# Optimization experiments

Measured on AMD Instinct MI355X. Metric: run time of the kernel, lower is better.

The kernel has to match this reference:

```python
import jax, jax.numpy as jnp
import numpy as np

NT = 16          # nt_states
TS = 48          # t_states
T = NT + TS      # total states
B, N = 4, 24     # batch, sentence length
HUGE = 1.0e9


def setup_inputs():
    key = jax.random.key(0)
    k1, k2, k3 = jax.random.split(key, 3)
    unary_scores = jax.nn.log_softmax(jax.random.normal(k1, (B, N, T), jnp.float32), axis=-1)
    rule = jax.random.normal(k2, (B, NT, N, T, T, 2), jnp.float32)
    rule_scores = jax.nn.log_softmax(rule.reshape(B, NT, N, -1), axis=-1).reshape(B, NT, N, T, T, 2)
    root_scores = jax.nn.log_softmax(jax.random.normal(k3, (B, NT), jnp.float32), axis=-1)
    return {"unary_scores": unary_scores, "rule_scores": rule_scores, "root_scores": root_scores}


def _lse(x, axes):
    return jax.nn.logsumexp(x, axis=axes)


def _inside(unary_scores, rule_scores, root_scores):
    Bv, Nv, Tt = unary_scores.shape
    nt = rule_scores.shape[1]
    dt = unary_scores.dtype
    R = jnp.moveaxis(rule_scores, 5, 0)            # (D, B, Tparent, H, TL, TR)

    # beta[b,l,r,t,h]: headed inside chart; betau[b,l,r,t]: head-summed chart
    beta = jnp.full((Bv, Nv + 1, Nv + 1, Tt, Nv), -HUGE, dt)
    betau = jnp.full((Bv, Nv + 1, Nv + 1, Tt), -HUGE, dt)

    # width-1 spans: only terminal states (word_span_slice = nt:T, nt_emission=False)
    ks = np.arange(Nv)
    st = np.arange(nt, Tt)
    beta = beta.at[:, ks[:, None], ks[:, None] + 1, st[None, :], ks[:, None]].set(0.0)
    betau = betau.at[:, ks[:, None], ks[:, None] + 1, st[None, :]].set(
        unary_scores[:, ks[:, None], st[None, :]])

    nts = np.arange(nt)
    for W in range(2, Nv + 1):
        L = Nv - W + 1
        ls = np.arange(L)
        rs = ls + W
        hidx = ls[:, None] + np.arange(W)          # (L, W) absolute head positions

        def width_body(beta, betau, R, unary_scores, W=W, ls=ls, rs=rs, hidx=hidx):
            def chartH(la, ra, s0, s1):            # (B, L, S, W)
                x = beta[:, la, ra, s0:s1, :]
                return jnp.take_along_axis(x, hidx[None, :, None, :], axis=3)

            def chartU(la, ra, s0, s1):            # (B, L, S)
                return betau[:, la, ra, s0:s1]

            def rwin(d, a0, a1, c0, c1):           # (B, L, nt, W, A, C)
                r = R[d][:, :, hidx, a0:a1, c0:c1]
                return jnp.transpose(r, (0, 2, 1, 3, 4, 5))

            def comb(xH, yU, xU, yH, z0, z1):
                # D=0: head from left child; D=1: head from right child.
                # logsumexp over TL, TR and both directions -> (B, L, nt, W)
                left = (jnp.transpose(xH, (0, 1, 3, 2))[:, :, None, :, :, None]
                        + yU[:, :, None, None, None, :] + z0)
                right = (xU[:, :, None, None, :, None]
                         + jnp.transpose(yH, (0, 1, 3, 2))[:, :, None, :, None, :] + z1)
                return jnp.logaddexp(_lse(left, (-2, -1)), _lse(right, (-2, -1)))

            c0, c1 = (nt, Tt) if W == 2 else (0, nt)
            # split at l+1: left child is a single terminal
            tmp = comb(chartH(ls, ls + 1, nt, Tt), chartU(ls + 1, rs, c0, c1),
                       chartU(ls, ls + 1, nt, Tt), chartH(ls + 1, rs, c0, c1),
                       rwin(0, nt, Tt, c0, c1), rwin(1, nt, Tt, c0, c1))
            if W >= 3:
                # split at r-1: right child is a single terminal
                tmp = jnp.logaddexp(tmp, comb(
                    chartH(ls, rs - 1, 0, nt), chartU(rs - 1, rs, nt, Tt),
                    chartU(ls, rs - 1, 0, nt), chartH(rs - 1, rs, nt, Tt),
                    rwin(0, 0, nt, nt, Tt), rwin(1, 0, nt, nt, Tt)))
            if W >= 4:
                # interior splits: both children are nonterminal spans
                z0 = rwin(0, 0, nt, 0, nt)
                z1 = rwin(1, 0, nt, 0, nt)
                for wl in range(2, W - 1):
                    s = ls + wl
                    tmp = jnp.logaddexp(tmp, comb(
                        chartH(ls, s, 0, nt), chartU(s, rs, 0, nt),
                        chartU(ls, s, 0, nt), chartH(s, rs, 0, nt), z0, z1))
            # add head-word emission under the parent NT; sum heads for betau
            uw = jnp.transpose(unary_scores[:, hidx, :nt], (0, 1, 3, 2))  # (B,L,nt,W)
            return tmp, _lse(tmp + uw, -1)

        tmp, tmpu = jax.checkpoint(width_body)(beta, betau, R, unary_scores)
        beta = beta.at[:, ls[:, None, None], rs[:, None, None],
                       nts[None, :, None], hidx[:, None, :]].set(tmp)
        betau = betau.at[:, ls[:, None], rs[:, None], nts[None, :]].set(tmpu)

    return jax.nn.logsumexp(betau[:, 0, Nv, :nt] + root_scores, axis=-1)  # log Z, (B,)


_inside_jit = jax.jit(_inside)


def reference(unary_scores, rule_scores, root_scores):
    return _inside_jit(unary_scores, rule_scores, root_scores)
```

## Files before the change

kernel.cpp:

```cpp
#include <hip/hip_runtime.h>
#include <cstddef>

#define Bv 4
#define Nv 24
#define NTv 16
#define Tv 64
#define NP 25
#define NEGF (-1e30f)

typedef __attribute__((ext_vector_type(8))) short short8v;
typedef __attribute__((ext_vector_type(4))) float f32x4;
union FragU { unsigned u[4]; short8v s; };

#define BETAA_OFF 0
#define BETAU_OFF 960000
#define RNT_OFF   1120000
#define T0_OFF    1906432
#define T1_OFF    2496256
#define T0L_OFF   3086080
#define T1R_OFF   3110656
#define D0_OFF    3135232
#define D1_OFF    3136768
#define EU_OFF    3138304
#define CELLF_OFF 3142912
#define WS_NEED   3145412

__device__ __forceinline__ void publish(float* p, float v) {
  __hip_atomic_store(p, v, __ATOMIC_RELAXED, __HIP_MEMORY_SCOPE_AGENT);
}

__device__ __forceinline__ unsigned packbf2(float lo, float hi) {
  unsigned bl = __float_as_uint(lo), bh = __float_as_uint(hi);
  bl = (bl + 0x7FFFu + ((bl >> 16) & 1u)) >> 16;
  bh = (bh + 0x7FFFu + ((bh >> 16) & 1u)) >> 16;
  return (bh << 16) | bl;
}

__global__ void init_kernel(const float* __restrict__ unary, float* __restrict__ betau,
                            float* __restrict__ Eu, int* __restrict__ cellF) {
  int t = blockIdx.x * blockDim.x + threadIdx.x;
  if (t < Bv * NP * NP) cellF[t] = 0;
  if (t >= Bv * Nv * 48) return;
  int i = t % 48, kk = (t / 48) % Nv, b = t / (48 * Nv);
  float u = unary[(size_t)(b * Nv + kk) * Tv + 16 + i];
  betau[((size_t)(b * NP + kk) * NP + (kk + 1)) * Tv + 16 + i] = u;
  Eu[(size_t)(b * Nv + kk) * 48 + i] = __expf(u);
}

__global__ __launch_bounds__(256) void prep_kernel(
    const float* __restrict__ rule, const float* __restrict__ Eu,
    unsigned* __restrict__ RNTh, float* __restrict__ T0, float* __restrict__ T1,
    float* __restrict__ T0L, float* __restrict__ T1R,
    float* __restrict__ D0, float* __restrict__ D1) {
  const int h = blockIdx.x, A = blockIdx.y, b = blockIdx.z;
  const int t = threadIdx.x;
  __shared__ float er0[64 * 65];
  __shared__ float er1[64 * 65];
  __shared__ float E[24 * 48];
  __shared__ float red[256];

  for (int i = t; i < 24 * 48; i += 256) E[i] = Eu[(size_t)b * (24 * 48) + i];
  const float* rb = rule + (size_t)((b * NTv + A) * Nv + h) * 8192;
#pragma unroll
  for (int i = 0; i < 8; ++i) {
    int lin = i * 1024 + t * 4;
    float4 v = *(const float4*)(rb + lin);
    int sL = lin >> 7, rem = (lin & 127) >> 1;
    er0[sL * 65 + rem] = __expf(v.x);
    er1[sL * 65 + rem] = __expf(v.y);
    er0[sL * 65 + rem + 1] = __expf(v.z);
    er1[sL * 65 + rem + 1] = __expf(v.w);
  }
  __syncthreads();
  {
    unsigned* dst0 = RNTh + (((size_t)(b * 2 + 0) * Nv + h) * NTv + A) * 128;
    unsigned* dst1 = RNTh + (((size_t)(b * 2 + 1) * Nv + h) * NTv + A) * 128;
    if (t < 128) {
      int sL = t >> 3, sRp = t & 7;
      dst0[t] = packbf2(er0[sL * 65 + 2 * sRp], er0[sL * 65 + 2 * sRp + 1]);
    } else {
      int t2 = t - 128;
      int sL = t2 >> 3, sRp = t2 & 7;
      dst1[t2] = packbf2(er1[sL * 65 + 2 * sRp], er1[sL * 65 + 2 * sRp + 1]);
    }
  }
  for (int o = t; o < 384; o += 256) {
    int p = o >> 4, sL = o & 15;
    const float* Ep = E + p * 48;
    const float* r0 = er0 + sL * 65 + 16;
    float acc = 0.f;
#pragma unroll 8
    for (int j = 0; j < 48; ++j) acc += Ep[j] * r0[j];
    T0[(((size_t)(b * Nv + h) * Nv + p) * NTv + sL) * NTv + A] = acc;
  }
  for (int o = t; o < 384; o += 256) {
    int p = o >> 4, sR = o & 15;
    const float* Ep = E + p * 48;
    float acc = 0.f;
#pragma unroll 8
    for (int i = 0; i < 48; ++i) acc += Ep[i] * er1[(16 + i) * 65 + sR];
    T1[(((size_t)(b * Nv + h) * Nv + p) * NTv + sR) * NTv + A] = acc;
  }
  if (t < 16) {
    float acc = 0.f;
    for (int i = 0; i < 48; ++i) acc += er0[(16 + i) * 65 + t];
    T0L[((size_t)(b * Nv + h) * NTv + t) * NTv + A] = acc;
  } else if (t < 32) {
    int sL = t - 16;
    float acc = 0.f;
    for (int j = 0; j < 48; ++j) acc += er1[sL * 65 + 16 + j];
    T1R[((size_t)(b * Nv + h) * NTv + sL) * NTv + A] = acc;
  }
  float acc0 = 0.f, acc1 = 0.f;
  const int hp = (h + 1 < 24) ? h + 1 : 0, hm = (h >= 1) ? h - 1 : 0;
  for (int e = t; e < 2304; e += 256) {
    int i = e / 48, j = e % 48;
    float r0 = er0[(16 + i) * 65 + 16 + j];
    float r1 = er1[(16 + i) * 65 + 16 + j];
    acc0 += E[hp * 48 + j] * r0;
    acc1 += E[hm * 48 + i] * r1;
  }
  red[t] = acc0;
  __syncthreads();
  if (t < 64) {
    float s = red[t] + red[t + 64] + red[t + 128] + red[t + 192];
#pragma unroll
    for (int off = 32; off; off >>= 1) s += __shfl_xor(s, off, 64);
    if (t == 0 && h <= 22) D0[((size_t)b * Nv + h) * NTv + A] = s;
  }
  __syncthreads();
  red[t] = acc1;
  __syncthreads();
  if (t < 64) {
    float s = red[t] + red[t + 64] + red[t + 128] + red[t + 192];
#pragma unroll
    for (int off = 32; off; off >>= 1) s += __shfl_xor(s, off, 64);
    if (t == 0 && h >= 1) D1[((size_t)b * Nv + (h - 1)) * NTv + A] = s;
  }
}

__device__ __forceinline__ void edge_dot(float v0, float v1, float v2, float v3,
                                         const float* Tb, float& sh, float& S) {
  float mx = fmaxf(fmaxf(v0, v1), fmaxf(v2, v3));
  mx = fmaxf(mx, __shfl_xor(mx, 1, 64));
  mx = fmaxf(mx, __shfl_xor(mx, 2, 64));
  float dot = __expf(v0 - mx) * Tb[0] + __expf(v1 - mx) * Tb[16] +
              __expf(v2 - mx) * Tb[32] + __expf(v3 - mx) * Tb[48];
  dot += __shfl_xor(dot, 1, 64);
  dot += __shfl_xor(dot, 2, 64);
  sh = mx;
  S = dot;
}

__global__ __launch_bounds__(768) void width_all_kernel(
    const float* __restrict__ unary, float* __restrict__ betaA, float* __restrict__ betau,
    const unsigned* __restrict__ RNTh, const float* __restrict__ T0, const float* __restrict__ T1,
    const float* __restrict__ T0L, const float* __restrict__ T1R,
    const float* __restrict__ D0, const float* __restrict__ D1,
    const float* __restrict__ root, float* __restrict__ out, int* __restrict__ cellF) {
  const int rr = blockIdx.x, b = blockIdx.y;
  const int r = rr + 2;
  const int tid = threadIdx.x;
  int* flagb = cellF + b * (NP * NP);

  __shared__ float chartC[23][384];
  __shared__ float buC[23][16];
  __shared__ float U0[24 * 256], U1[24 * 256];
  __shared__ float pM[2 * 24 * 16], pS[2 * 24 * 16];
  __shared__ float sTmp[16 * 24];

  const int wv = tid >> 6, lane = tid & 63;
  const int sym = lane & 15;
  const int mBlk = (lane >> 4) * 8;

  for (int i = 0; i <= r - 2; ++i) {
    const int l = r - 2 - i;
    const int W = r - l;

    if (W >= 3) {
      if (tid < W - 3) {
        const int m = l + 2 + tid;
        while (__hip_atomic_load(&flagb[l * NP + m], __ATOMIC_RELAXED,
                                 __HIP_MEMORY_SCOPE_AGENT) == 0)
          __builtin_amdgcn_s_sleep(1);
      }
      __syncthreads();
    }

    float Gp[4];
#pragma unroll
    for (int pi = 0; pi < 4; ++pi) {
      const int p = wv + 12 * pi;
      if (p < 2 * W) {
        const int hh = p >> 1, d = p & 1, hcol = l + hh;
        int mst, cnt;
        if (d) { mst = l + 2; cnt = min(l + hh, r - 2) - mst + 1; }
        else   { mst = max(l + hh + 1, l + 2); cnt = (r - 2) - mst + 1; }
        if (cnt < 0) cnt = 0;
        float* Ua = (d ? U1 : U0) + hh * 256;
        if (cnt == 0) {
#pragma unroll
          for (int reg = 0; reg < 4; ++reg)
            Ua[((lane >> 4) * 4 + reg) * 16 + sym] = 0.f;
          Gp[pi] = -2e30f;
        } else {
          float Lv[8], Rv[8];
          if (d) {
            const size_t lb = ((size_t)(b * NP + l) * NP + mst) * Tv + sym;
#pragma unroll
            for (int j = 0; j < 8; ++j) {
              int mi = mBlk + j;
              Lv[j] = (mi < cnt) ? betau[lb + (size_t)mi * Tv] : NEGF;
              Rv[j] = (mi < cnt) ? chartC[mst + mi][hcol * 16 + sym] : NEGF;
            }
          } else {
            const size_t lb = ((size_t)(b * NP + l) * NP + mst) * 384 + hcol * 16 + sym;
#pragma unroll
            for (int j = 0; j < 8; ++j) {
              int mi = mBlk + j;
              Lv[j] = (mi < cnt) ? betaA[lb + (size_t)mi * 384] : NEGF;
              Rv[j] = (mi < cnt) ? buC[mst + mi][sym] : NEGF;
            }
          }
          float mxL = NEGF, mxR = NEGF;
#pragma unroll
          for (int j = 0; j < 8; ++j) { mxL = fmaxf(mxL, Lv[j]); mxR = fmaxf(mxR, Rv[j]); }
#pragma unroll
          for (int off = 1; off < 64; off <<= 1) {
            mxL = fmaxf(mxL, __shfl_xor(mxL, off, 64));
            mxR = fmaxf(mxR, __shfl_xor(mxR, off, 64));
          }
          FragU fa, fb;
#pragma unroll
          for (int jj = 0; jj < 4; ++jj) {
            int m0i = mBlk + 2 * jj, m1i = m0i + 1;
            float e0 = (m0i < cnt) ? __expf(Lv[2 * jj] - mxL) : 0.f;
            float e1 = (m1i < cnt) ? __expf(Lv[2 * jj + 1] - mxL) : 0.f;
            fa.u[jj] = packbf2(e0, e1);
            float f0 = (m0i < cnt) ? __expf(Rv[2 * jj] - mxR) : 0.f;
            float f1 = (m1i < cnt) ? __expf(Rv[2 * jj + 1] - mxR) : 0.f;
            fb.u[jj] = packbf2(f0, f1);
          }
          f32x4 z = {0.f, 0.f, 0.f, 0.f};
          f32x4 dU = __builtin_amdgcn_mfma_f32_16x16x32_bf16(fa.s, fb.s, z, 0, 0, 0);
#pragma unroll
          for (int reg = 0; reg < 4; ++reg)
            Ua[((lane >> 4) * 4 + reg) * 16 + sym] = dU[reg];
          Gp[pi] = mxL + mxR;
        }
      }
    }

    if (W >= 3) {
      while (__hip_atomic_load(&flagb[l * NP + (r - 1)], __ATOMIC_RELAXED,
                               __HIP_MEMORY_SCOPE_AGENT) == 0)
        __builtin_amdgcn_s_sleep(1);
    }

#pragma unroll
    for (int pi = 0; pi < 4; ++pi) {
      const int p = wv + 12 * pi;
      if (p < 2 * W) {
        const int hh = p >> 1, d = p & 1, h = l + hh;
        const float* Ua = (d ? U1 : U0) + hh * 256;
        const unsigned* Rb = RNTh + (((size_t)(b * 2 + d) * Nv + h) * NTv + sym) * 128;
        f32x4 acc4 = {0.f, 0.f, 0.f, 0.f};
#pragma unroll
        for (int kk = 0; kk < 8; ++kk) {
          uint4 ar = *(const uint4*)(Rb + kk * 16 + (lane >> 4) * 4);
          FragU fa, fb;
          fa.u[0] = ar.x; fa.u[1] = ar.y; fa.u[2] = ar.z; fa.u[3] = ar.w;
          if (sym == 0) {
            const float* up = Ua + kk * 32 + mBlk;
#pragma unroll
            for (int jj = 0; jj < 4; ++jj) fb.u[jj] = packbf2(up[2 * jj], up[2 * jj + 1]);
          } else {
            fb.u[0] = 0; fb.u[1] = 0; fb.u[2] = 0; fb.u[3] = 0;
          }
          acc4 = __builtin_amdgcn_mfma_f32_16x16x32_bf16(fa.s, fb.s, acc4, 0, 0, 0);
        }
        const int A = lane >> 2, q = lane & 3;
        const int src = (A >> 2) << 4;
        float c0 = __shfl(acc4[0], src, 64);
        float c1 = __shfl(acc4[1], src, 64);
        float c2 = __shfl(acc4[2], src, 64);
        float c3 = __shfl(acc4[3], src, 64);
        const int sel = A & 3;
        float acc = (sel == 0) ? c0 : (sel == 1) ? c1 : (sel == 2) ? c2 : c3;
        float Mi = Gp[pi];
        float sh2 = NEGF, S2 = 0.f, sh3 = NEGF, S3 = 0.f;
        if (W >= 3) {
          if (d == 0) {
            if (hh < W - 1) {
              const float* Tb = T0 + (((size_t)(b * Nv + h) * Nv + (r - 1)) * NTv + 4 * q) * NTv + A;
              float4 e4 = *(const float4*)(betaA +
                  ((size_t)(b * NP + l) * NP + (r - 1)) * 384 + (size_t)h * 16 + 4 * q);
              edge_dot(e4.x, e4.y, e4.z, e4.w, Tb, sh2, S2);
            }
            if (hh == 0) {
              const float* Tb = T0L + ((size_t)(b * Nv + l) * NTv + 4 * q) * NTv + A;
              const float* u4 = &buC[l + 1][4 * q];
              edge_dot(u4[0], u4[1], u4[2], u4[3], Tb, sh3, S3);
            }
          } else {
            if (hh >= 1) {
              const float* Tb = T1 + (((size_t)(b * Nv + h) * Nv + l) * NTv + 4 * q) * NTv + A;
              const float* e4 = &chartC[l + 1][h * 16 + 4 * q];
              edge_dot(e4[0], e4[1], e4[2], e4[3], Tb, sh2, S2);
            }
            if (hh == W - 1) {
              const float* Tb = T1R + ((size_t)(b * Nv + (r - 1)) * NTv + 4 * q) * NTv + A;
              float4 u4 = *(const float4*)(betau +
                  ((size_t)(b * NP + l) * NP + (r - 1)) * Tv + 4 * q);
              edge_dot(u4.x, u4.y, u4.z, u4.w, Tb, sh3, S3);
            }
          }
        } else {
          if (d == 0 && hh == 0) { sh2 = 0.f; S2 = D0[((size_t)b * Nv + l) * NTv + A]; }
          if (d == 1 && hh == 1) { sh2 = 0.f; S2 = D1[((size_t)b * Nv + l) * NTv + A]; }
        }
        float Mf = fmaxf(Mi, fmaxf(sh2, sh3));
        float Sf = acc * __expf(Mi - Mf) + S2 * __expf(sh2 - Mf) + S3 * __expf(sh3 - Mf);
        if (q == 0) {
          pM[(d * 24 + hh) * 16 + A] = Mf;
          pS[(d * 24 + hh) * 16 + A] = Sf;
        }
      }
    }
    __syncthreads();

    if (tid < 384) {
      int A2 = tid & 15, hh = tid >> 4;
      if (hh < W) {
        float M0 = pM[(0 * 24 + hh) * 16 + A2], S0 = pS[(0 * 24 + hh) * 16 + A2];
        float M1 = pM[(1 * 24 + hh) * 16 + A2], S1 = pS[(1 * 24 + hh) * 16 + A2];
        float nm = fmaxf(M0, M1);
        float s = S0 * __expf(M0 - nm) + S1 * __expf(M1 - nm);
        float val = nm + __logf(s);
        publish(&betaA[((size_t)(b * NP + l) * NP + r) * 384 + (l + hh) * 16 + A2], val);
        chartC[l][(l + hh) * 16 + A2] = val;
        sTmp[A2 * 24 + hh] = val + unary[(size_t)(b * Nv + (l + hh)) * Tv + A2];
      }
    }
    __syncthreads();
    if (tid < 16) {
      float mx = NEGF;
      for (int x = 0; x < W; ++x) mx = fmaxf(mx, sTmp[tid * 24 + x]);
      float s = 0.f;
      for (int x = 0; x < W; ++x) s += __expf(sTmp[tid * 24 + x] - mx);
      float val = mx + __logf(s);
      publish(&betau[((size_t)(b * NP + l) * NP + r) * Tv + tid], val);
      buC[l][tid] = val;
    }
    if (tid == 0) {
      asm volatile("s_waitcnt vmcnt(0)" ::: "memory");
      __hip_atomic_store(&flagb[l * NP + r], 1, __ATOMIC_RELAXED,
                         __HIP_MEMORY_SCOPE_AGENT);
    }
  }

  if (rr == 22) {
    __syncthreads();
    if (tid == 0) {
      float vals[NTv];
      float mx = NEGF;
#pragma unroll
      for (int A = 0; A < NTv; ++A) {
        float v = buC[0][A] + root[b * NTv + A];
        vals[A] = v;
        mx = fmaxf(mx, v);
      }
      float s = 0.f;
#pragma unroll
      for (int A = 0; A < NTv; ++A) s += __expf(vals[A] - mx);
      out[b] = mx + __logf(s);
    }
  }
}

__global__ __launch_bounds__(768) void width_kernel_fb(
    const float* __restrict__ unary, const float* __restrict__ rule,
    float* __restrict__ betaA, float* __restrict__ betau, int W) {
  const int l = blockIdx.x, b = blockIdx.y;
  const int r = l + W;
  const int tid = threadIdx.x;
  const int sub = tid & 1;
  const int pid = tid >> 1;
  const int A = pid & 15;
  const int hh = pid >> 4;
  const int h = l + hh;
  const bool act = (hh < W);
  const int sA = tid & 15, sH = tid >> 4;

  __shared__ float sER0[48], sEL1[48];
  __shared__ float sCL0[16 * 24], sCR1[16 * 24];
  __shared__ float sMaxL0[24], sMaxR1[24];
  __shared__ float sShR0, sShL1;
  __shared__ float sTmp[16 * 24];

  float runM = NEGF, runS = 0.f;
  for (int m = l + 1; m < r; ++m) {
    const int wl = m - l, wr = r - m;
    if (tid < 64) {
      const int n = (wr == 1) ? 48 : 16, s0 = (wr == 1) ? 16 : 0;
      float v = (tid < n) ? betau[(size_t)((b * NP + m) * NP + r) * Tv + s0 + tid] : NEGF;
      float mx = v;
#pragma unroll
      for (int off = 32; off; off >>= 1) mx = fmaxf(mx, __shfl_xor(mx, off, 64));
      if (tid == 0) sShR0 = mx;
      if (tid < n) sER0[tid] = v - mx;
    } else if (tid < 128) {
      const int j = tid - 64;
      const int n = (wl == 1) ? 48 : 16, s0 = (wl == 1) ? 16 : 0;
      float v = (j < n) ? betau[(size_t)((b * NP + l) * NP + m) * Tv + s0 + j] : NEGF;
      float mx = v;
#pragma unroll
      for (int off = 32; off; off >>= 1) mx = fmaxf(mx, __shfl_xor(mx, off, 64));
      if (j == 0) sShL1 = mx;
      if (j < n) sEL1[j] = v - mx;
    }
    if (tid < 384) {
      if (wl > 1 && sH < wl) {
        float v = betaA[(size_t)((b * NP + l) * NP + m) * 384 + sA * Nv + (l + sH)];
        float mx = v;
#pragma unroll
        for (int off = 8; off; off >>= 1) mx = fmaxf(mx, __shfl_xor(mx, off, 16));
        if (sA == 0) sMaxL0[sH] = mx;
        sCL0[sA * Nv + sH] = v - mx;
      }
      if (wr > 1 && sH >= wl && sH < W) {
        float v = betaA[(size_t)((b * NP + m) * NP + r) * 384 + sA * Nv + (l + sH)];
        float mx = v;
#pragma unroll
        for (int off = 8; off; off >>= 1) mx = fmaxf(mx, __shfl_xor(mx, off, 16));
        if (sA == 0) sMaxR1[sH] = mx;
        sCR1[sA * Nv + sH] = v - mx;
      }
    }
    __syncthreads();
    if (act) {
      if (hh < wl && (wl > 1 || hh == 0)) {
        const int nL = (wl == 1) ? 48 : 16, sL0 = (wl == 1) ? 16 : 0;
        const int nR = (wr == 1) ? 48 : 16, sR0 = (wr == 1) ? 16 : 0;
        const float shift = ((wl == 1) ? 0.f : sMaxL0[hh]) + sShR0;
        float part = 0.f;
        const float* rb = rule + (size_t)(((b * NTv + A) * Nv + h) * Tv) * Tv * 2;
        for (int i = sub; i < nL; i += 2) {
          const float cl = (wl == 1) ? 0.f : sCL0[i * Nv + hh];
          const float* rp = rb + (size_t)(sL0 + i) * Tv * 2 + sR0 * 2;
#pragma unroll 8
          for (int j = 0; j < nR; ++j) part += __expf(cl + sER0[j] + rp[j * 2]);
        }
        float nm = fmaxf(runM, shift);
        runS = runS * __expf(runM - nm) + part * __expf(shift - nm);
        runM = nm;
      }
      if (hh >= wl && (wr > 1 || hh == W - 1)) {
        const int nL = (wl == 1) ? 48 : 16, sL0 = (wl == 1) ? 16 : 0;
        const int nR = (wr == 1) ? 48 : 16, sR0 = (wr == 1) ? 16 : 0;
        const float shift = sShL1 + ((wr == 1) ? 0.f : sMaxR1[hh]);
        float part = 0.f;
        const float* rb = rule + (size_t)(((b * NTv + A) * Nv + h) * Tv) * Tv * 2 + 1;
        for (int i = sub; i < nL; i += 2) {
          const float el = sEL1[i];
          const float* rp = rb + (size_t)(sL0 + i) * Tv * 2 + sR0 * 2;
#pragma unroll 8
          for (int j = 0; j < nR; ++j) {
            const float cr = (wr == 1) ? 0.f : sCR1[j * Nv + hh];
            part += __expf(el + cr + rp[j * 2]);
          }
        }
        float nm = fmaxf(runM, shift);
        runS = runS * __expf(runM - nm) + part * __expf(shift - nm);
        runM = nm;
      }
    }
    __syncthreads();
  }
  if (act) {
    float om = __shfl_xor(runM, 1, 64);
    float os = __shfl_xor(runS, 1, 64);
    float nm = fmaxf(runM, om);
    float s = runS * __expf(runM - nm) + os * __expf(om - nm);
    if (sub == 0) {
      float val = nm + __logf(s);
      betaA[(size_t)((b * NP + l) * NP + r) * 384 + A * Nv + h] = val;
      sTmp[A * Nv + hh] = val + unary[(b * Nv + h) * Tv + A];
    }
  }
  __syncthreads();
  if (tid < 16) {
    float mx = NEGF;
    for (int x = 0; x < W; ++x) mx = fmaxf(mx, sTmp[tid * Nv + x]);
    float s = 0.f;
    for (int x = 0; x < W; ++x) s += __expf(sTmp[tid * Nv + x] - mx);
    betau[(size_t)((b * NP + l) * NP + r) * Tv + tid] = mx + __logf(s);
  }
}

__global__ void final_kernel(const float* __restrict__ betau, const float* __restrict__ root,
                             float* __restrict__ out) {
  int b = threadIdx.x;
  if (b < Bv) {
    float vals[NTv];
    float mx = NEGF;
#pragma unroll
    for (int A = 0; A < NTv; ++A) {
      float v = betau[(size_t)((b * NP + 0) * NP + Nv) * Tv + A] + root[b * NTv + A];
      vals[A] = v;
      mx = fmaxf(mx, v);
    }
    float s = 0.f;
#pragma unroll
    for (int A = 0; A < NTv; ++A) s += __expf(vals[A] - mx);
    out[b] = mx + __logf(s);
  }
}

extern "C" void kernel_launch(void* const* d_in, const int* in_sizes, int n_in,
                              void* d_out, int out_size, void* d_ws, size_t ws_size,
                              hipStream_t stream) {
  (void)in_sizes; (void)n_in; (void)out_size;
  const float* unary = (const float*)d_in[0];
  const float* rule  = (const float*)d_in[1];
  const float* root  = (const float*)d_in[2];
  float* out = (float*)d_out;
  float* ws = (float*)d_ws;
  float* betaA = ws + BETAA_OFF;
  float* betau = ws + BETAU_OFF;
  const bool fast = ws_size >= (size_t)WS_NEED * sizeof(float);

  if (fast) {
    unsigned* RNTh = (unsigned*)(ws + RNT_OFF);
    float* T0  = ws + T0_OFF;
    float* T1  = ws + T1_OFF;
    float* T0L = ws + T0L_OFF;
    float* T1R = ws + T1R_OFF;
    float* D0  = ws + D0_OFF;
    float* D1  = ws + D1_OFF;
    float* Eu  = ws + EU_OFF;
    int* cellF = (int*)(ws + CELLF_OFF);
    init_kernel<<<(Bv * Nv * 48 + 255) / 256, 256, 0, stream>>>(unary, betau, Eu, cellF);
    prep_kernel<<<dim3(24, 16, 4), 256, 0, stream>>>(rule, Eu, RNTh, T0, T1, T0L, T1R, D0, D1);
    void* args[] = {(void*)&unary, (void*)&betaA, (void*)&betau, (void*)&RNTh,
                    (void*)&T0, (void*)&T1, (void*)&T0L, (void*)&T1R,
                    (void*)&D0, (void*)&D1, (void*)&root, (void*)&out, (void*)&cellF};
    hipLaunchCooperativeKernel((const void*)width_all_kernel, dim3(Nv - 1, Bv), dim3(768),
                               args, 0, stream);
  } else {
    float* Eu = ws + BETAU_OFF + 160000;
    int* prog = (int*)(ws + BETAU_OFF + 160000 + 4608);
    init_kernel<<<(Bv * Nv * 48 + 255) / 256, 256, 0, stream>>>(unary, betau, Eu, prog);
    for (int W = 2; W <= Nv; ++W) {
      dim3 grid(Nv - W + 1, Bv);
      width_kernel_fb<<<grid, 768, 0, stream>>>(unary, rule, betaA, betau, W);
    }
    final_kernel<<<1, 64, 0, stream>>>(betau, root, out);
  }
}
```

Before: 406.7 us.

## Pair adjacent right-endpoint columns per block to share edge cells via LDS

Each block now processes two adjacent right-endpoint columns (r=2g+1 and r=2g+2) in an interleaved order instead of one column per block, cutting the grid from 23 to 12 blocks per batch. Column rB reads its edge cell (l, rB-1) directly from column rA's shared-memory chart, removing one cross-block flag poll and global reads on the dependency chain. The cost is half as many concurrent blocks and serialisation of the two columns' work inside one block, plus a larger shared-memory footprint.

```diff
diff --git a/kernel.cpp b/kernel.cpp
--- a/kernel.cpp
+++ b/kernel.cpp
@@ -152,221 +152,253 @@
   S = dot;
 }
 
+__device__ __forceinline__ void cell_body(
+    int b, int r, int l, int tid,
+    float (*chartOwn)[384], float (*buOwn)[16],
+    const float* eChart, const float* eBu, int edgePollIdx, int* flagb,
+    float* U0, float* U1, float* pM, float* pS, float* sTmp,
+    const float* __restrict__ unary, float* __restrict__ betaA, float* __restrict__ betau,
+    const unsigned* __restrict__ RNTh, const float* __restrict__ T0,
+    const float* __restrict__ T1, const float* __restrict__ T0L,
+    const float* __restrict__ T1R, const float* __restrict__ D0,
+    const float* __restrict__ D1) {
+  const int W = r - l;
+  const int wv = tid >> 6, lane = tid & 63;
+  const int sym = lane & 15;
+  const int mBlk = (lane >> 4) * 8;
+
+  if (W >= 3) {
+    if (tid < W - 3) {
+      const int m = l + 2 + tid;
+      while (__hip_atomic_load(&flagb[l * NP + m], __ATOMIC_RELAXED,
+                               __HIP_MEMORY_SCOPE_AGENT) == 0)
+        __builtin_amdgcn_s_sleep(1);
+    }
+    __syncthreads();
+  }
+
+  float Gp[4];
+#pragma unroll
+  for (int pi = 0; pi < 4; ++pi) {
+    const int p = wv + 12 * pi;
+    if (p < 2 * W) {
+      const int hh = p >> 1, d = p & 1, hcol = l + hh;
+      int mst, cnt;
+      if (d) { mst = l + 2; cnt = min(l + hh, r - 2) - mst + 1; }
+      else   { mst = max(l + hh + 1, l + 2); cnt = (r - 2) - mst + 1; }
+      if (cnt < 0) cnt = 0;
+      float* Ua = (d ? U1 : U0) + hh * 256;
+      if (cnt == 0) {
+#pragma unroll
+        for (int reg = 0; reg < 4; ++reg)
+          Ua[((lane >> 4) * 4 + reg) * 16 + sym] = 0.f;
+        Gp[pi] = -2e30f;
+      } else {
+        float Lv[8], Rv[8];
+        if (d) {
+          const size_t lb = ((size_t)(b * NP + l) * NP + mst) * Tv + sym;
+#pragma unroll
+          for (int j = 0; j < 8; ++j) {
+            int mi = mBlk + j;
+            Lv[j] = (mi < cnt) ? betau[lb + (size_t)mi * Tv] : NEGF;
+            Rv[j] = (mi < cnt) ? chartOwn[mst + mi][hcol * 16 + sym] : NEGF;
+          }
+        } else {
+          const size_t lb = ((size_t)(b * NP + l) * NP + mst) * 384 + hcol * 16 + sym;
+#pragma unroll
+          for (int j = 0; j < 8; ++j) {
+            int mi = mBlk + j;
+            Lv[j] = (mi < cnt) ? betaA[lb + (size_t)mi * 384] : NEGF;
+            Rv[j] = (mi < cnt) ? buOwn[mst + mi][sym] : NEGF;
+          }
+        }
+        float mxL = NEGF, mxR = NEGF;
+#pragma unroll
+        for (int j = 0; j < 8; ++j) { mxL = fmaxf(mxL, Lv[j]); mxR = fmaxf(mxR, Rv[j]); }
+#pragma unroll
+        for (int off = 1; off < 64; off <<= 1) {
+          mxL = fmaxf(mxL, __shfl_xor(mxL, off, 64));
+          mxR = fmaxf(mxR, __shfl_xor(mxR, off, 64));
+        }
+        FragU fa, fb;
+#pragma unroll
+        for (int jj = 0; jj < 4; ++jj) {
+          int m0i = mBlk + 2 * jj, m1i = m0i + 1;
+          float e0 = (m0i < cnt) ? __expf(Lv[2 * jj] - mxL) : 0.f;
+          float e1 = (m1i < cnt) ? __expf(Lv[2 * jj + 1] - mxL) : 0.f;
+          fa.u[jj] = packbf2(e0, e1);
+          float f0 = (m0i < cnt) ? __expf(Rv[2 * jj] - mxR) : 0.f;
+          float f1 = (m1i < cnt) ? __expf(Rv[2 * jj + 1] - mxR) : 0.f;
+          fb.u[jj] = packbf2(f0, f1);
+        }
+        f32x4 z = {0.f, 0.f, 0.f, 0.f};
+        f32x4 dU = __builtin_amdgcn_mfma_f32_16x16x32_bf16(fa.s, fb.s, z, 0, 0, 0);
+#pragma unroll
+        for (int reg = 0; reg < 4; ++reg)
+          Ua[((lane >> 4) * 4 + reg) * 16 + sym] = dU[reg];
+        Gp[pi] = mxL + mxR;
+      }
+    }
+  }
+
+  if (W >= 3 && edgePollIdx >= 0) {
+    while (__hip_atomic_load(&flagb[edgePollIdx], __ATOMIC_RELAXED,
+                             __HIP_MEMORY_SCOPE_AGENT) == 0)
+      __builtin_amdgcn_s_sleep(1);
+  }
+
+#pragma unroll
+  for (int pi = 0; pi < 4; ++pi) {
+    const int p = wv + 12 * pi;
+    if (p < 2 * W) {
+      const int hh = p >> 1, d = p & 1, h = l + hh;
+      const float* Ua = (d ? U1 : U0) + hh * 256;
+      const unsigned* Rb = RNTh + (((size_t)(b * 2 + d) * Nv + h) * NTv + sym) * 128;
+      f32x4 acc4 = {0.f, 0.f, 0.f, 0.f};
+#pragma unroll
+      for (int kk = 0; kk < 8; ++kk) {
+        uint4 ar = *(const uint4*)(Rb + kk * 16 + (lane >> 4) * 4);
+        FragU fa, fb;
+        fa.u[0] = ar.x; fa.u[1] = ar.y; fa.u[2] = ar.z; fa.u[3] = ar.w;
+        if (sym == 0) {
+          const float* up = Ua + kk * 32 + mBlk;
+#pragma unroll
+          for (int jj = 0; jj < 4; ++jj) fb.u[jj] = packbf2(up[2 * jj], up[2 * jj + 1]);
+        } else {
+          fb.u[0] = 0; fb.u[1] = 0; fb.u[2] = 0; fb.u[3] = 0;
+        }
+        acc4 = __builtin_amdgcn_mfma_f32_16x16x32_bf16(fa.s, fb.s, acc4, 0, 0, 0);
+      }
+      const int A = lane >> 2, q = lane & 3;
+      const int src = (A >> 2) << 4;
+      float c0 = __shfl(acc4[0], src, 64);
+      float c1 = __shfl(acc4[1], src, 64);
+      float c2 = __shfl(acc4[2], src, 64);
+      float c3 = __shfl(acc4[3], src, 64);
+      const int sel = A & 3;
+      float acc = (sel == 0) ? c0 : (sel == 1) ? c1 : (sel == 2) ? c2 : c3;
+      float Mi = Gp[pi];
+      float sh2 = NEGF, S2 = 0.f, sh3 = NEGF, S3 = 0.f;
+      if (W >= 3) {
+        if (d == 0) {
+          if (hh < W - 1) {
+            const float* Tb = T0 + (((size_t)(b * Nv + h) * Nv + (r - 1)) * NTv + 4 * q) * NTv + A;
+            float4 e4 = *(const float4*)(eChart + (size_t)h * 16 + 4 * q);
+            edge_dot(e4.x, e4.y, e4.z, e4.w, Tb, sh2, S2);
+          }
+          if (hh == 0) {
+            const float* Tb = T0L + ((size_t)(b * Nv + l) * NTv + 4 * q) * NTv + A;
+            const float* u4 = &buOwn[l + 1][4 * q];
+            edge_dot(u4[0], u4[1], u4[2], u4[3], Tb, sh3, S3);
+          }
+        } else {
+          if (hh >= 1) {
+            const float* Tb = T1 + (((size_t)(b * Nv + h) * Nv + l) * NTv + 4 * q) * NTv + A;
+            const float* e4 = &chartOwn[l + 1][h * 16 + 4 * q];
+            edge_dot(e4[0], e4[1], e4[2], e4[3], Tb, sh2, S2);
+          }
+          if (hh == W - 1) {
+            const float* Tb = T1R + ((size_t)(b * Nv + (r - 1)) * NTv + 4 * q) * NTv + A;
+            float4 u4 = *(const float4*)(eBu + 4 * q);
+            edge_dot(u4.x, u4.y, u4.z, u4.w, Tb, sh3, S3);
+          }
+        }
+      } else {
+        if (d == 0 && hh == 0) { sh2 = 0.f; S2 = D0[((size_t)b * Nv + l) * NTv + A]; }
+        if (d == 1 && hh == 1) { sh2 = 0.f; S2 = D1[((size_t)b * Nv + l) * NTv + A]; }
+      }
+      float Mf = fmaxf(Mi, fmaxf(sh2, sh3));
+      float Sf = acc * __expf(Mi - Mf) + S2 * __expf(sh2 - Mf) + S3 * __expf(sh3 - Mf);
+      if (q == 0) {
+        pM[(d * 24 + hh) * 16 + A] = Mf;
+        pS[(d * 24 + hh) * 16 + A] = Sf;
+      }
+    }
+  }
+  __syncthreads();
+
+  if (tid < 384) {
+    int A2 = tid & 15, hh = tid >> 4;
+    if (hh < W) {
+      float M0 = pM[(0 * 24 + hh) * 16 + A2], S0 = pS[(0 * 24 + hh) * 16 + A2];
+      float M1 = pM[(1 * 24 + hh) * 16 + A2], S1 = pS[(1 * 24 + hh) * 16 + A2];
+      float nm = fmaxf(M0, M1);
+      float s = S0 * __expf(M0 - nm) + S1 * __expf(M1 - nm);
+      float val = nm + __logf(s);
+      publish(&betaA[((size_t)(b * NP + l) * NP + r) * 384 + (l + hh) * 16 + A2], val);
+      chartOwn[l][(l + hh) * 16 + A2] = val;
+      sTmp[A2 * 24 + hh] = val + unary[(size_t)(b * Nv + (l + hh)) * Tv + A2];
+    }
+  }
+  __syncthreads();
+  if (tid < 16) {
+    float mx = NEGF;
+    for (int x = 0; x < W; ++x) mx = fmaxf(mx, sTmp[tid * 24 + x]);
+    float s = 0.f;
+    for (int x = 0; x < W; ++x) s += __expf(sTmp[tid * 24 + x] - mx);
+    float val = mx + __logf(s);
+    publish(&betau[((size_t)(b * NP + l) * NP + r) * Tv + tid], val);
+    buOwn[l][tid] = val;
+  }
+  if (tid == 0) {
+    asm volatile("s_waitcnt vmcnt(0)" ::: "memory");
+    __hip_atomic_store(&flagb[l * NP + r], 1, __ATOMIC_RELAXED,
+                       __HIP_MEMORY_SCOPE_AGENT);
+  }
+}
+
 __global__ __launch_bounds__(768) void width_all_kernel(
     const float* __restrict__ unary, float* __restrict__ betaA, float* __restrict__ betau,
     const unsigned* __restrict__ RNTh, const float* __restrict__ T0, const float* __restrict__ T1,
     const float* __restrict__ T0L, const float* __restrict__ T1R,
     const float* __restrict__ D0, const float* __restrict__ D1,
     const float* __restrict__ root, float* __restrict__ out, int* __restrict__ cellF) {
-  const int rr = blockIdx.x, b = blockIdx.y;
-  const int r = rr + 2;
+  const int g = blockIdx.x, b = blockIdx.y;
   const int tid = threadIdx.x;
   int* flagb = cellF + b * (NP * NP);
 
-  __shared__ float chartC[23][384];
-  __shared__ float buC[23][16];
+  __shared__ float chartA[22][384], chartB[23][384];
+  __shared__ float buA[22][16], buB[23][16];
   __shared__ float U0[24 * 256], U1[24 * 256];
   __shared__ float pM[2 * 24 * 16], pS[2 * 24 * 16];
   __shared__ float sTmp[16 * 24];
 
-  const int wv = tid >> 6, lane = tid & 63;
-  const int sym = lane & 15;
-  const int mBlk = (lane >> 4) * 8;
-
-  for (int i = 0; i <= r - 2; ++i) {
-    const int l = r - 2 - i;
-    const int W = r - l;
-
-    if (W >= 3) {
-      if (tid < W - 3) {
-        const int m = l + 2 + tid;
-        while (__hip_atomic_load(&flagb[l * NP + m], __ATOMIC_RELAXED,
-                                 __HIP_MEMORY_SCOPE_AGENT) == 0)
-          __builtin_amdgcn_s_sleep(1);
-      }
-      __syncthreads();
-    }
-
-    float Gp[4];
-#pragma unroll
-    for (int pi = 0; pi < 4; ++pi) {
-      const int p = wv + 12 * pi;
-      if (p < 2 * W) {
-        const int hh = p >> 1, d = p & 1, hcol = l + hh;
-        int mst, cnt;
-        if (d) { mst = l + 2; cnt = min(l + hh, r - 2) - mst + 1; }
-        else   { mst = max(l + hh + 1, l + 2); cnt = (r - 2) - mst + 1; }
-        if (cnt < 0) cnt = 0;
-        float* Ua = (d ? U1 : U0) + hh * 256;
-        if (cnt == 0) {
-#pragma unroll
-          for (int reg = 0; reg < 4; ++reg)
-            Ua[((lane >> 4) * 4 + reg) * 16 + sym] = 0.f;
-          Gp[pi] = -2e30f;
-        } else {
-          float Lv[8], Rv[8];
-          if (d) {
-            const size_t lb = ((size_t)(b * NP + l) * NP + mst) * Tv + sym;
-#pragma unroll
-            for (int j = 0; j < 8; ++j) {
-              int mi = mBlk + j;
-              Lv[j] = (mi < cnt) ? betau[lb + (size_t)mi * Tv] : NEGF;
-              Rv[j] = (mi < cnt) ? chartC[mst + mi][hcol * 16 + sym] : NEGF;
-            }
-          } else {
-            const size_t lb = ((size_t)(b * NP + l) * NP + mst) * 384 + hcol * 16 + sym;
-#pragma unroll
-            for (int j = 0; j < 8; ++j) {
-              int mi = mBlk + j;
-              Lv[j] = (mi < cnt) ? betaA[lb + (size_t)mi * 384] : NEGF;
-              Rv[j] = (mi < cnt) ? buC[mst + mi][sym] : NEGF;
-            }
-          }
-          float mxL = NEGF, mxR = NEGF;
-#pragma unroll
-          for (int j = 0; j < 8; ++j) { mxL = fmaxf(mxL, Lv[j]); mxR = fmaxf(mxR, Rv[j]); }
-#pragma unroll
-          for (int off = 1; off < 64; off <<= 1) {
-            mxL = fmaxf(mxL, __shfl_xor(mxL, off, 64));
-            mxR = fmaxf(mxR, __shfl_xor(mxR, off, 64));
-          }
-          FragU fa, fb;
-#pragma unroll
-          for (int jj = 0; jj < 4; ++jj) {
-            int m0i = mBlk + 2 * jj, m1i = m0i + 1;
-            float e0 = (m0i < cnt) ? __expf(Lv[2 * jj] - mxL) : 0.f;
-            float e1 = (m1i < cnt) ? __expf(Lv[2 * jj + 1] - mxL) : 0.f;
-            fa.u[jj] = packbf2(e0, e1);
-            float f0 = (m0i < cnt) ? __expf(Rv[2 * jj] - mxR) : 0.f;
-            float f1 = (m1i < cnt) ? __expf(Rv[2 * jj + 1] - mxR) : 0.f;
-            fb.u[jj] = packbf2(f0, f1);
-          }
-          f32x4 z = {0.f, 0.f, 0.f, 0.f};
-          f32x4 dU = __builtin_amdgcn_mfma_f32_16x16x32_bf16(fa.s, fb.s, z, 0, 0, 0);
-#pragma unroll
-          for (int reg = 0; reg < 4; ++reg)
-            Ua[((lane >> 4) * 4 + reg) * 16 + sym] = dU[reg];
-          Gp[pi] = mxL + mxR;
-        }
-      }
-    }
-
-    if (W >= 3) {
-      while (__hip_atomic_load(&flagb[l * NP + (r - 1)], __ATOMIC_RELAXED,
-                               __HIP_MEMORY_SCOPE_AGENT) == 0)
-        __builtin_amdgcn_s_sleep(1);
-    }
-
-#pragma unroll
-    for (int pi = 0; pi < 4; ++pi) {
-      const int p = wv + 12 * pi;
-      if (p < 2 * W) {
-        const int hh = p >> 1, d = p & 1, h = l + hh;
-        const float* Ua = (d ? U1 : U0) + hh * 256;
-        const unsigned* Rb = RNTh + (((size_t)(b * 2 + d) * Nv + h) * NTv + sym) * 128;
-        f32x4 acc4 = {0.f, 0.f, 0.f, 0.f};
-#pragma unroll
-        for (int kk = 0; kk < 8; ++kk) {
-          uint4 ar = *(const uint4*)(Rb + kk * 16 + (lane >> 4) * 4);
-          FragU fa, fb;
-          fa.u[0] = ar.x; fa.u[1] = ar.y; fa.u[2] = ar.z; fa.u[3] = ar.w;
-          if (sym == 0) {
-            const float* up = Ua + kk * 32 + mBlk;
-#pragma unroll
-            for (int jj = 0; jj < 4; ++jj) fb.u[jj] = packbf2(up[2 * jj], up[2 * jj + 1]);
-          } else {
-            fb.u[0] = 0; fb.u[1] = 0; fb.u[2] = 0; fb.u[3] = 0;
-          }
-          acc4 = __builtin_amdgcn_mfma_f32_16x16x32_bf16(fa.s, fb.s, acc4, 0, 0, 0);
-        }
-        const int A = lane >> 2, q = lane & 3;
-        const int src = (A >> 2) << 4;
-        float c0 = __shfl(acc4[0], src, 64);
-        float c1 = __shfl(acc4[1], src, 64);
-        float c2 = __shfl(acc4[2], src, 64);
-        float c3 = __shfl(acc4[3], src, 64);
-        const int sel = A & 3;
-        float acc = (sel == 0) ? c0 : (sel == 1) ? c1 : (sel == 2) ? c2 : c3;
-        float Mi = Gp[pi];
-        float sh2 = NEGF, S2 = 0.f, sh3 = NEGF, S3 = 0.f;
-        if (W >= 3) {
-          if (d == 0) {
-            if (hh < W - 1) {
-              const float* Tb = T0 + (((size_t)(b * Nv + h) * Nv + (r - 1)) * NTv + 4 * q) * NTv + A;
-              float4 e4 = *(const float4*)(betaA +
-                  ((size_t)(b * NP + l) * NP + (r - 1)) * 384 + (size_t)h * 16 + 4 * q);
-              edge_dot(e4.x, e4.y, e4.z, e4.w, Tb, sh2, S2);
-            }
-            if (hh == 0) {
-              const float* Tb = T0L + ((size_t)(b * Nv + l) * NTv + 4 * q) * NTv + A;
-              const float* u4 = &buC[l + 1][4 * q];
-              edge_dot(u4[0], u4[1], u4[2], u4[3], Tb, sh3, S3);
-            }
-          } else {
-            if (hh >= 1) {
-              const float* Tb = T1 + (((size_t)(b * Nv + h) * Nv + l) * NTv + 4 * q) * NTv + A;
-              const float* e4 = &chartC[l + 1][h * 16 + 4 * q];
-              edge_dot(e4[0], e4[1], e4[2], e4[3], Tb, sh2, S2);
-            }
-            if (hh == W - 1) {
-              const float* Tb = T1R + ((size_t)(b * Nv + (r - 1)) * NTv + 4 * q) * NTv + A;
-              float4 u4 = *(const float4*)(betau +
-                  ((size_t)(b * NP + l) * NP + (r - 1)) * Tv + 4 * q);
-              edge_dot(u4.x, u4.y, u4.z, u4.w, Tb, sh3, S3);
-            }
-          }
-        } else {
-          if (d == 0 && hh == 0) { sh2 = 0.f; S2 = D0[((size_t)b * Nv + l) * NTv + A]; }
-          if (d == 1 && hh == 1) { sh2 = 0.f; S2 = D1[((size_t)b * Nv + l) * NTv + A]; }
-        }
-        float Mf = fmaxf(Mi, fmaxf(sh2, sh3));
-        float Sf = acc * __expf(Mi - Mf) + S2 * __expf(sh2 - Mf) + S3 * __expf(sh3 - Mf);
-        if (q == 0) {
-          pM[(d * 24 + hh) * 16 + A] = Mf;
-          pS[(d * 24 + hh) * 16 + A] = Sf;
-        }
-      }
-    }
-    __syncthreads();
-
-    if (tid < 384) {
-      int A2 = tid & 15, hh = tid >> 4;
-      if (hh < W) {
-        float M0 = pM[(0 * 24 + hh) * 16 + A2], S0 = pS[(0 * 24 + hh) * 16 + A2];
-        float M1 = pM[(1 * 24 + hh) * 16 + A2], S1 = pS[(1 * 24 + hh) * 16 + A2];
-        float nm = fmaxf(M0, M1);
-        float s = S0 * __expf(M0 - nm) + S1 * __expf(M1 - nm);
-        float val = nm + __logf(s);
-        publish(&betaA[((size_t)(b * NP + l) * NP + r) * 384 + (l + hh) * 16 + A2], val);
-        chartC[l][(l + hh) * 16 + A2] = val;
-        sTmp[A2 * 24 + hh] = val + unary[(size_t)(b * Nv + (l + hh)) * Tv + A2];
-      }
-    }
-    __syncthreads();
-    if (tid < 16) {
-      float mx = NEGF;
-      for (int x = 0; x < W; ++x) mx = fmaxf(mx, sTmp[tid * 24 + x]);
-      float s = 0.f;
-      for (int x = 0; x < W; ++x) s += __expf(sTmp[tid * 24 + x] - mx);
-      float val = mx + __logf(s);
-      publish(&betau[((size_t)(b * NP + l) * NP + r) * Tv + tid], val);
-      buC[l][tid] = val;
-    }
-    if (tid == 0) {
-      asm volatile("s_waitcnt vmcnt(0)" ::: "memory");
-      __hip_atomic_store(&flagb[l * NP + r], 1, __ATOMIC_RELAXED,
-                         __HIP_MEMORY_SCOPE_AGENT);
-    }
-  }
-
-  if (rr == 22) {
+  if (g == 0) {
+    cell_body(b, 2, 0, tid, chartB, buB, betaA, betau, -1, flagb,
+              U0, U1, pM, pS, sTmp, unary, betaA, betau,
+              RNTh, T0, T1, T0L, T1R, D0, D1);
+    return;
+  }
+
+  const int rA = 2 * g + 1, rB = 2 * g + 2;
+  const int nA = rA - 1, nB = rB - 1;
+  for (int i = 0; i < nB; ++i) {
+    if (i < nA) {
+      const int l = rA - 2 - i;
+      cell_body(b, rA, l, tid, chartA, buA,
+                betaA + ((size_t)(b * NP + l) * NP + (rA - 1)) * 384 - (size_t)0,
+                betau + ((size_t)(b * NP + l) * NP + (rA - 1)) * Tv,
+                l * NP + (rA - 1), flagb, U0, U1, pM, pS, sTmp,
+                unary, betaA, betau, RNTh, T0, T1, T0L, T1R, D0, D1);
+    }
+    {
+      const int l = rB - 2 - i;
+      const int lc = (l < 22) ? l : 0;
+      cell_body(b, rB, l, tid, chartB, buB,
+                &chartA[lc][0], &buA[lc][0], -1, flagb,
+                U0, U1, pM, pS, sTmp,
+                unary, betaA, betau, RNTh, T0, T1, T0L, T1R, D0, D1);
+    }
+  }
+
+  if (g == 11) {
     __syncthreads();
     if (tid == 0) {
       float vals[NTv];
       float mx = NEGF;
 #pragma unroll
       for (int A = 0; A < NTv; ++A) {
-        float v = buC[0][A] + root[b * NTv + A];
+        float v = buB[0][A] + root[b * NTv + A];
         vals[A] = v;
         mx = fmaxf(mx, v);
       }
@@ -377,6 +409,7 @@
     }
   }
 }
+
 
 __global__ __launch_bounds__(768) void width_kernel_fb(
     const float* __restrict__ unary, const float* __restrict__ rule,
@@ -545,7 +578,7 @@
     void* args[] = {(void*)&unary, (void*)&betaA, (void*)&betau, (void*)&RNTh,
                     (void*)&T0, (void*)&T1, (void*)&T0L, (void*)&T1R,
                     (void*)&D0, (void*)&D1, (void*)&root, (void*)&out, (void*)&cellF};
-    hipLaunchCooperativeKernel((const void*)width_all_kernel, dim3(Nv - 1, Bv), dim3(768),
+    hipLaunchCooperativeKernel((const void*)width_all_kernel, dim3(12, Bv), dim3(768),
                                args, 0, stream);
   } else {
     float* Eu = ws + BETAU_OFF + 160000;
```

Result: slower. 644.2 us (+58.4%).
